# Kernel optimization log

Measured on AMD Instinct MI355X. Metric: run time of the kernel, lower is better.

## Reference

```python
import jax, jax.numpy as jnp
import numpy as np

H = 128; L = 4; N_TOTAL = 2500; M = 4; K = 12
S = N_TOTAL * M          # 10000 subgraphs
F = S * K                # 120000 flat nodes
E_INTRA = 2 * F          # 240000 intra-subgraph edges
E_INTER = 16 * N_TOTAL   # 40000 canonical edges
B = 50; VOCAB = 119; MAX_DIST = 32; BN_EPS = 1e-5


def _bn(x, g, b):
    # training-mode BatchNorm1d over rows (biased var, eps=1e-5)
    mu = x.mean(0)
    var = x.var(0)
    return (x - mu) * jax.lax.rsqrt(var + BN_EPS) * g + b


def _gine(x, ei, ea, W1, b1, W2, b2):
    # PyG GINEConv, eps=0: MLP(x + sum_{src->dst} relu(x[src] + e))
    msg = jax.nn.relu(x[ei[0]] + ea)                              # [E,H]
    agg = jax.ops.segment_sum(msg, ei[1], num_segments=x.shape[0])
    h = x + agg
    return jax.nn.relu(h @ W1 + b1) @ W2 + b2


def setup_inputs():
    key = jax.random.key(0)
    ks = list(jax.random.split(key, 32)); it = iter(ks)
    nk = lambda: next(it)
    rn = lambda shape, s=0.05: jax.random.normal(nk(), shape, dtype=jnp.float32) * s
    x_tok = jax.random.randint(nk(), (F,), 0, VOCAB)
    dist = jax.random.randint(nk(), (F,), 0, MAX_DIST + 1)
    node_ids = jax.random.randint(nk(), (F,), 0, N_TOTAL)
    node_ids = jnp.where(jax.random.uniform(nk(), (F,)) < 0.1, -1, node_ids)
    root_flat_idx = jnp.arange(S) * K
    node_ids = node_ids.at[root_flat_idx].set(jnp.arange(S) // M)  # root = canonical node
    valid = node_ids >= 0
    sub_batch = jnp.repeat(jnp.arange(S), K)
    src = jax.random.randint(nk(), (E_INTRA,), 0, F)
    dst = (src // K) * K + jax.random.randint(nk(), (E_INTRA,), 0, K)  # stay inside subgraph
    intra_ei = jnp.stack([src, dst])
    edge_index = jax.random.randint(nk(), (2, E_INTER), 0, N_TOTAL)
    batch_ids = jnp.arange(N_TOTAL) // (N_TOTAL // B)
    lp = -jax.random.uniform(nk(), (S,)) * 3.0                    # log-probs <= 0
    z = lambda *shape: jnp.zeros(shape, jnp.float32)
    o = lambda *shape: jnp.ones(shape, jnp.float32)
    return dict(
        x_tok=x_tok, dist=dist, node_ids=node_ids, valid=valid,
        sub_batch=sub_batch, root_flat_idx=root_flat_idx,
        intra_ei=intra_ei, edge_index=edge_index, batch_ids=batch_ids,
        lp=lp, ea_flat=rn((E_INTRA, H)), edge_attr=rn((E_INTER, H)),
        atom_emb=rn((VOCAB, H)), dist_emb=rn((MAX_DIST + 1, H)),
        logp_w=rn((1, H)), logp_b=z(H),
        intra_W1=rn((L, H, H)), intra_b1=z(L, H),
        intra_W2=rn((L, H, H)), intra_b2=z(L, H),
        intra_bn_g=o(L, H), intra_bn_b=z(L, H),
        self_W=rn((L, H, H)), self_b=z(L, H),
        root_W=rn((L, H, H)), root_b=z(L, H),
        inter_W1=rn((L, H, H)), inter_b1=z(L, H),
        inter_W2=rn((L, H, H)), inter_b2=z(L, H),
        inter_bn_g=o(L, H), inter_bn_b=z(L, H),
        readout_bn_g=o(H), readout_bn_b=z(H),
        alpha_pool=o(1), alpha_inter=o(1),
    )


def reference(x_tok, dist, node_ids, valid, sub_batch, root_flat_idx, intra_ei,
              edge_index, batch_ids, lp, ea_flat, edge_attr, atom_emb, dist_emb,
              logp_w, logp_b, intra_W1, intra_b1, intra_W2, intra_b2,
              intra_bn_g, intra_bn_b, self_W, self_b, root_W, root_b,
              inter_W1, inter_b1, inter_W2, inter_b2, inter_bn_g, inter_bn_b,
              readout_bn_g, readout_bn_b, alpha_pool, alpha_inter):
    valid_f = valid.astype(jnp.float32)[:, None]                  # [F,1]
    is_root_f = jnp.zeros((F, 1), jnp.float32).at[root_flat_idx].set(1.0)
    clamped_ids = jnp.maximum(node_ids, 0)
    # input encoding: atom embedding + BFS-distance PE + log-prob PE
    logp_pe = jax.nn.relu(lp[sub_batch][:, None] * logp_w[0] + logp_b)
    h = (atom_emb[x_tok] + dist_emb[dist] + logp_pe) * valid_f
    # HT inter-root weights, normalized per canonical root id
    root_ids = node_ids[root_flat_idx]                            # [S]
    rv = root_ids >= 0
    rid = jnp.maximum(root_ids, 0)
    w_un = jnp.where(rv, jnp.exp(-alpha_inter[0] * lp), 0.0)
    w_sum = jax.ops.segment_sum(w_un, rid, num_segments=N_TOTAL)
    ht_w = jnp.where(rv, w_un / (w_sum[rid] + 1e-16), 0.0)        # [S]
    for l in range(L):
        h1 = _gine(h, intra_ei, ea_flat, intra_W1[l], intra_b1[l], intra_W2[l], intra_b2[l])
        h1 = _bn(h1, intra_bn_g[l], intra_bn_b[l]) * valid_f
        h_root_bcast = h[sub_batch * K]
        h_non_root = (h @ self_W[l] + self_b[l]) + (h_root_bcast @ root_W[l] + root_b[l])
        # HT-weighted scatter of root reps to canonical nodes
        h_roots = h[root_flat_idx]                                # [S,H]
        h_root_canon = jax.ops.segment_sum(h_roots * ht_w[:, None], rid, num_segments=N_TOTAL)
        h_inter = _gine(h_root_canon, edge_index, edge_attr, inter_W1[l], inter_b1[l], inter_W2[l], inter_b2[l])
        h_inter = _bn(h_inter, inter_bn_g[l], inter_bn_b[l])
        h_inter_bcast = h_inter[clamped_ids] * valid_f
        out = is_root_f * (h1 + h_inter_bcast) + (1.0 - is_root_f) * (h1 + h_non_root)
        h = jax.nn.relu(out) * valid_f                            # dropout p=0
    # HT softmax readout over the m subgraphs of each canonical node
    h_sub = jax.ops.segment_sum(h * valid_f, sub_batch, num_segments=S)
    h_sub_2d = h_sub.reshape(N_TOTAL, M, H)
    w = jax.nn.softmax(-alpha_pool[0] * lp.reshape(N_TOTAL, M), axis=1)
    node_emb = jnp.einsum('nm,nmh->nh', w, h_sub_2d)
    node_emb = _bn(node_emb, readout_bn_g, readout_bn_b)
    return jax.ops.segment_sum(node_emb, batch_ids, num_segments=B)  # [B,H]
```

## Files before the change

### kernel.cpp

```cpp
#include <hip/hip_runtime.h>
#include <math.h>

#define H 128
#define H4 (H/4)
#define KK 12
#define MSUB 4
#define FF 120000
#define SS 10000
#define NN 2500
#define NBATCH 50
#define NLAYER 4
#define EINTRA 240000
#define EINTER 40000
#define HH (H*H)
#define BN_EPS 1e-5f
#define CAP_I 32
#define CAP_E 96
#define WLO_SHORTS 16384

typedef short short8 __attribute__((ext_vector_type(8)));
typedef float floatx4 __attribute__((ext_vector_type(4)));

__device__ __forceinline__ unsigned short f2bf_rne(float x){
  unsigned u = __float_as_uint(x);
  unsigned r = u + 0x7FFFu + ((u >> 16) & 1u);
  return (unsigned short)(r >> 16);
}


__global__ void k_zeroi(int* __restrict__ p, int n){
  int i = blockIdx.x*256 + threadIdx.x;
  if (i < n) p[i] = 0;
}


__global__ void k_bucket(const int* __restrict__ dst, int E, int* __restrict__ cnt,
                         int* __restrict__ beid, int cap){
  int e = blockIdx.x*256 + threadIdx.x;
  if (e >= E) return;
  int d = dst[e];
  int p = atomicAdd(&cnt[d], 1);
  if (p < cap) beid[(size_t)d*cap + p] = e;
}

__global__ void k_scan(const int* __restrict__ cnt, int rows, int cap,
                       int* __restrict__ rowptr, int* __restrict__ gcount){
  __shared__ int sdata[256];
  __shared__ int sbase;
  int tid = threadIdx.x;
  int r = blockIdx.x*256 + tid;
  int v = 0;
  if (r < rows){ v = cnt[r]; if (v > cap) v = cap; }
  sdata[tid] = v;
  __syncthreads();
  for (int ofs = 1; ofs < 256; ofs <<= 1){
    int t = (tid >= ofs) ? sdata[tid-ofs] : 0;
    __syncthreads();
    sdata[tid] += t;
    __syncthreads();
  }
  if (tid == 255) sbase = atomicAdd(gcount, sdata[255]);
  __syncthreads();
  if (r < rows) rowptr[r] = sbase + sdata[tid] - v;
}

__global__ void k_csr_fill(const int* __restrict__ cnt, const int* __restrict__ rowptr,
                           const int* __restrict__ beid, const int* __restrict__ src,
                           int rows, int cap, int2* __restrict__ es){
  int f = blockIdx.x*256 + threadIdx.x;
  if (f >= rows) return;
  int n = cnt[f]; if (n > cap) n = cap;
  int base = rowptr[f];
  const int* bl = beid + (size_t)f*cap;
  for (int i = 0; i < n; ++i){
    int e = bl[i];
    es[base + i] = make_int2(e, src[e]);
  }
}


__global__ void k_wprep(const float* __restrict__ iW1, const float* __restrict__ iW2,
                        const float* __restrict__ sW,  const float* __restrict__ rW,
                        const float* __restrict__ nW1, const float* __restrict__ nW2,
                        short* __restrict__ wlo){
  int mat = blockIdx.x >> 3;
  int t = (blockIdx.x & 7)*256 + threadIdx.x;
  int l = t & 63, nt = (t >> 6) & 7, ks = t >> 9;
  int layer = mat / 6, which = mat % 6;
  const float* W;
  switch (which){
    case 0: W = iW1; break; case 1: W = iW2; break; case 2: W = sW; break;
    case 3: W = rW;  break; case 4: W = nW1; break; default: W = nW2; break;
  }
  W += (size_t)layer*HH;
  short* o = wlo + (size_t)mat*WLO_SHORTS;
  int quad = l >> 4, n15 = l & 15;
  #pragma unroll
  for (int j = 0; j < 8; ++j){
    int k = ks*32 + quad*8 + j;
    int n = nt*16 + n15;
    float v = W[(size_t)k*H + n];
    unsigned short hb = f2bf_rne(v);
    float hf = __uint_as_float((unsigned)hb << 16);
    o[(ks*8 + nt)*512 + l*8 + j] = (short)f2bf_rne(v - hf);
  }
}


__global__ void k_encode(float* __restrict__ h, const int* __restrict__ xtok,
                         const int* __restrict__ dist, const int* __restrict__ nids,
                         const int* __restrict__ subb, const float* __restrict__ lp,
                         const float* __restrict__ aemb, const float* __restrict__ demb,
                         const float* __restrict__ lw, const float* __restrict__ lb){
  int idx = blockIdx.x*256 + threadIdx.x;
  if (idx >= FF*H4) return;
  int f = idx >> 5; int c = (idx & 31) << 2;
  float vf = (nids[f] >= 0) ? 1.f : 0.f;
  float l = lp[subb[f]];
  float4 a = *(const float4*)(aemb + (size_t)xtok[f]*H + c);
  float4 d = *(const float4*)(demb + (size_t)dist[f]*H + c);
  float4 w = *(const float4*)(lw + c);
  float4 b = *(const float4*)(lb + c);
  float4 o;
  o.x = (a.x + d.x + fmaxf(fmaf(l, w.x, b.x), 0.f)) * vf;
  o.y = (a.y + d.y + fmaxf(fmaf(l, w.y, b.y), 0.f)) * vf;
  o.z = (a.z + d.z + fmaxf(fmaf(l, w.z, b.z), 0.f)) * vf;
  o.w = (a.w + d.w + fmaxf(fmaf(l, w.w, b.w), 0.f)) * vf;
  *(float4*)(h + (size_t)f*H + c) = o;
}


__global__ void k_htw(const int* __restrict__ nids, const int* __restrict__ rfi,
                      const float* __restrict__ lp, const float* __restrict__ alpha,
                      float* __restrict__ htw){
  int n = blockIdx.x*256 + threadIdx.x;
  if (n >= NN) return;
  float a = alpha[0];
  float w[MSUB]; float sum = 0.f;
  #pragma unroll
  for (int m = 0; m < MSUB; ++m){
    int s = n*MSUB + m;
    int rid = nids[rfi[s]];
    float wm = (rid >= 0) ? expf(-a*lp[s]) : 0.f;
    w[m] = wm; sum += wm;
  }
  float inv = 1.f / (sum + 1e-16f);
  #pragma unroll
  for (int m = 0; m < MSUB; ++m) htw[n*MSUB + m] = w[m]*inv;
}


__global__ void k_gine_gather2(float* __restrict__ outa, const float* __restrict__ x,
                               const float* __restrict__ ea, const int* __restrict__ cnt,
                               const int* __restrict__ rowptr, const int2* __restrict__ es,
                               int rows, int cap){
  int idx = blockIdx.x*256 + threadIdx.x;
  if (idx >= rows*H4) return;
  int f = idx >> 5; int c = (idx & 31) << 2;
  float4 acc = *(const float4*)(x + (size_t)f*H + c);
  int n = cnt[f]; if (n > cap) n = cap;
  const int2* p = es + rowptr[f];
  int i = 0;
  for (; i + 2 <= n; i += 2){
    int2 e0 = p[i];
    int2 e1 = p[i+1];
    float4 x0 = *(const float4*)(x + (size_t)e0.y*H + c);
    float4 a0 = *(const float4*)(ea + (size_t)e0.x*H + c);
    float4 x1 = *(const float4*)(x + (size_t)e1.y*H + c);
    float4 a1 = *(const float4*)(ea + (size_t)e1.x*H + c);
    acc.x += fmaxf(x0.x + a0.x, 0.f) + fmaxf(x1.x + a1.x, 0.f);
    acc.y += fmaxf(x0.y + a0.y, 0.f) + fmaxf(x1.y + a1.y, 0.f);
    acc.z += fmaxf(x0.z + a0.z, 0.f) + fmaxf(x1.z + a1.z, 0.f);
    acc.w += fmaxf(x0.w + a0.w, 0.f) + fmaxf(x1.w + a1.w, 0.f);
  }
  if (i < n){
    int2 e0 = p[i];
    float4 x0 = *(const float4*)(x + (size_t)e0.y*H + c);
    float4 a0 = *(const float4*)(ea + (size_t)e0.x*H + c);
    acc.x += fmaxf(x0.x + a0.x, 0.f);
    acc.y += fmaxf(x0.y + a0.y, 0.f);
    acc.z += fmaxf(x0.z + a0.z, 0.f);
    acc.w += fmaxf(x0.w + a0.w, 0.f);
  }
  *(float4*)(outa + (size_t)f*H + c) = acc;
}


__global__ void k_canon(float* __restrict__ canon, const float* __restrict__ h,
                        const float* __restrict__ htw, const int* __restrict__ rfi){
  int idx = blockIdx.x*256 + threadIdx.x;
  if (idx >= NN*H4) return;
  int n = idx >> 5; int c = (idx & 31) << 2;
  float4 acc = make_float4(0.f,0.f,0.f,0.f);
  #pragma unroll
  for (int m = 0; m < MSUB; ++m){
    int s = n*MSUB + m;
    float w = htw[s];
    const float* p = h + (size_t)rfi[s]*H + c;
    acc.x += w*p[0]; acc.y += w*p[1]; acc.z += w*p[2]; acc.w += w*p[3];
  }
  *(float4*)(canon + (size_t)n*H + c) = acc;
}


__global__ __launch_bounds__(256, 2) void k_mm_mfma(
    const float* __restrict__ in, float* __restrict__ out, int rows,
    const float* __restrict__ W, const short* __restrict__ wlo,
    const float* __restrict__ bias, int do_relu, const int* __restrict__ gather)
{
  __shared__ __align__(16) short whi[4][8][64][8];
  int tid = threadIdx.x;
  int w = tid >> 6, l = tid & 63;
  int quad = l >> 4, n15 = l & 15;

  #pragma unroll
  for (int i = 0; i < 8; ++i){
    int c = w + (i << 2);
    int ks = c >> 3, nt = c & 7;
    #pragma unroll
    for (int j = 0; j < 8; ++j){
      int k = ks*32 + quad*8 + j;
      int n = nt*16 + n15;
      whi[ks][nt][l][j] = (short)f2bf_rne(W[(size_t)k*H + n]);
    }
  }
  __syncthreads();

  const short* wlol = wlo + l*8;

  int ngroups = (rows + 63) >> 6;
  for (int g = blockIdx.x; g < ngroups; g += gridDim.x){
    int rload = g*64 + w*16 + n15;
    bool okload = rload < rows;
    int ir = okload ? (gather ? gather[rload] : rload) : 0;
    const float* ap = in + (size_t)ir*H + quad*8;

    short8 ah[4], al[4];
    #pragma unroll
    for (int ks = 0; ks < 4; ++ks){
      float4 a0 = okload ? *(const float4*)(ap + ks*32 + 0) : make_float4(0.f,0.f,0.f,0.f);
      float4 a1 = okload ? *(const float4*)(ap + ks*32 + 4) : make_float4(0.f,0.f,0.f,0.f);
      float av[8] = {a0.x,a0.y,a0.z,a0.w,a1.x,a1.y,a1.z,a1.w};
      #pragma unroll
      for (int j = 0; j < 8; ++j){
        unsigned short hb = f2bf_rne(av[j]);
        float hf = __uint_as_float((unsigned)hb << 16);
        ah[ks][j] = (short)hb;
        al[ks][j] = (short)f2bf_rne(av[j] - hf);
      }
    }

    floatx4 acc[8] = {};
    #pragma unroll
    for (int ks = 0; ks < 4; ++ks){
      #pragma unroll
      for (int nt = 0; nt < 8; ++nt){
        short8 bh = *(const short8*)&whi[ks][nt][l][0];
        short8 bl = *(const short8*)(wlol + (ks*8 + nt)*512);
        acc[nt] = __builtin_amdgcn_mfma_f32_16x16x32_bf16(ah[ks], bh, acc[nt], 0, 0, 0);
        acc[nt] = __builtin_amdgcn_mfma_f32_16x16x32_bf16(al[ks], bh, acc[nt], 0, 0, 0);
        acc[nt] = __builtin_amdgcn_mfma_f32_16x16x32_bf16(ah[ks], bl, acc[nt], 0, 0, 0);
      }
    }

    int rbase = g*64 + w*16 + quad*4;
    #pragma unroll
    for (int nt = 0; nt < 8; ++nt){
      int col = nt*16 + n15;
      float bv = bias[col];
      #pragma unroll
      for (int reg = 0; reg < 4; ++reg){
        int r = rbase + reg;
        if (r < rows){
          float v = acc[nt][reg] + bv;
          if (do_relu) v = fmaxf(v, 0.f);
          out[(size_t)r*H + col] = v;
        }
      }
    }
  }
}


__global__ __launch_bounds__(256, 2) void k_mm_mfma_stats(
    const float* __restrict__ in, float* __restrict__ out, int rows,
    const float* __restrict__ W, const short* __restrict__ wlo,
    const float* __restrict__ bias, double* __restrict__ part)
{
  __shared__ __align__(16) short whi[4][8][64][8];
  int tid = threadIdx.x;
  int w = tid >> 6, l = tid & 63;
  int quad = l >> 4, n15 = l & 15;

  #pragma unroll
  for (int i = 0; i < 8; ++i){
    int c = w + (i << 2);
    int ks = c >> 3, nt = c & 7;
    #pragma unroll
    for (int j = 0; j < 8; ++j){
      int k = ks*32 + quad*8 + j;
      int n = nt*16 + n15;
      whi[ks][nt][l][j] = (short)f2bf_rne(W[(size_t)k*H + n]);
    }
  }
  __syncthreads();

  const short* wlol = wlo + l*8;

  float s0[8] = {0,0,0,0,0,0,0,0};
  float s1[8] = {0,0,0,0,0,0,0,0};

  int ngroups = (rows + 63) >> 6;
  for (int g = blockIdx.x; g < ngroups; g += gridDim.x){
    int rload = g*64 + w*16 + n15;
    bool okload = rload < rows;
    const float* ap = in + (size_t)(okload ? rload : 0)*H + quad*8;

    short8 ah[4], al[4];
    #pragma unroll
    for (int ks = 0; ks < 4; ++ks){
      float4 a0 = okload ? *(const float4*)(ap + ks*32 + 0) : make_float4(0.f,0.f,0.f,0.f);
      float4 a1 = okload ? *(const float4*)(ap + ks*32 + 4) : make_float4(0.f,0.f,0.f,0.f);
      float av[8] = {a0.x,a0.y,a0.z,a0.w,a1.x,a1.y,a1.z,a1.w};
      #pragma unroll
      for (int j = 0; j < 8; ++j){
        unsigned short hb = f2bf_rne(av[j]);
        float hf = __uint_as_float((unsigned)hb << 16);
        ah[ks][j] = (short)hb;
        al[ks][j] = (short)f2bf_rne(av[j] - hf);
      }
    }

    floatx4 acc[8] = {};
    #pragma unroll
    for (int ks = 0; ks < 4; ++ks){
      #pragma unroll
      for (int nt = 0; nt < 8; ++nt){
        short8 bh = *(const short8*)&whi[ks][nt][l][0];
        short8 bl = *(const short8*)(wlol + (ks*8 + nt)*512);
        acc[nt] = __builtin_amdgcn_mfma_f32_16x16x32_bf16(ah[ks], bh, acc[nt], 0, 0, 0);
        acc[nt] = __builtin_amdgcn_mfma_f32_16x16x32_bf16(al[ks], bh, acc[nt], 0, 0, 0);
        acc[nt] = __builtin_amdgcn_mfma_f32_16x16x32_bf16(ah[ks], bl, acc[nt], 0, 0, 0);
      }
    }

    int rbase = g*64 + w*16 + quad*4;
    #pragma unroll
    for (int nt = 0; nt < 8; ++nt){
      int col = nt*16 + n15;
      float bv = bias[col];
      #pragma unroll
      for (int reg = 0; reg < 4; ++reg){
        int r = rbase + reg;
        if (r < rows){
          float v = acc[nt][reg] + bv;
          out[(size_t)r*H + col] = v;
          s0[nt] += v;
          s1[nt] += v*v;
        }
      }
    }
  }

  __syncthreads();
  double* red = (double*)&whi[0][0][0][0];
  #pragma unroll
  for (int nt = 0; nt < 8; ++nt){
    float a = s0[nt], b = s1[nt];
    a += __shfl_xor(a, 16, 64); b += __shfl_xor(b, 16, 64);
    a += __shfl_xor(a, 32, 64); b += __shfl_xor(b, 32, 64);
    if (quad == 0){
      int col = nt*16 + n15;
      red[(size_t)(w*2+0)*H + col] = (double)a;
      red[(size_t)(w*2+1)*H + col] = (double)b;
    }
  }
  __syncthreads();
  if (tid < H){
    int col = tid;
    double a = red[0*H+col] + red[2*H+col] + red[4*H+col] + red[6*H+col];
    double b = red[1*H+col] + red[3*H+col] + red[5*H+col] + red[7*H+col];
    part[(size_t)(blockIdx.x*2+0)*H + col] = a;
    part[(size_t)(blockIdx.x*2+1)*H + col] = b;
  }
}


__global__ void k_bnstats_p(const float* __restrict__ x, int rows, double* __restrict__ part){
  int g = blockIdx.x*256 + threadIdx.x;
  int c = g & (H-1);
  int s = g >> 7;
  int stride = (gridDim.x*256) >> 7;
  double a = 0.0, b = 0.0;
  for (int r = s; r < rows; r += stride){
    float v = x[(size_t)r*H + c];
    a += v; b += (double)v*(double)v;
  }
  part[(size_t)(s*2+0)*H + c] = a;
  part[(size_t)(s*2+1)*H + c] = b;
}

__global__ void k_bnfin_par(const double* __restrict__ part, int nstreams, int rows,
                            float* __restrict__ muinv){
  __shared__ double sh0[256], sh1[256];
  int c = blockIdx.x;
  int tid = threadIdx.x;
  double a = 0.0, b = 0.0;
  for (int s = tid; s < nstreams; s += 256){
    a += part[(size_t)(s*2+0)*H + c];
    b += part[(size_t)(s*2+1)*H + c];
  }
  sh0[tid] = a; sh1[tid] = b;
  __syncthreads();
  for (int ofs = 128; ofs > 0; ofs >>= 1){
    if (tid < ofs){ sh0[tid] += sh0[tid+ofs]; sh1[tid] += sh1[tid+ofs]; }
    __syncthreads();
  }
  if (tid == 0){
    double mu = sh0[0] / (double)rows;
    double var = sh1[0] / (double)rows - mu*mu;
    muinv[c]   = (float)mu;
    muinv[H+c] = (float)(1.0 / sqrt(var + (double)BN_EPS));
  }
}

__global__ void k_bnapply(float* __restrict__ x, const float* __restrict__ muinv,
                          const float* __restrict__ g, const float* __restrict__ b, int rows){
  int idx = blockIdx.x*256 + threadIdx.x;
  if (idx >= rows*H4) return;
  int r = idx >> 5; int c = (idx & 31) << 2;
  float4 v  = *(const float4*)(x + (size_t)r*H + c);
  float4 mu = *(const float4*)(muinv + c);
  float4 iv = *(const float4*)(muinv + H + c);
  float4 gg = *(const float4*)(g + c);
  float4 bb = *(const float4*)(b + c);
  v.x = (v.x-mu.x)*iv.x*gg.x + bb.x;
  v.y = (v.y-mu.y)*iv.y*gg.y + bb.y;
  v.z = (v.z-mu.z)*iv.z*gg.z + bb.z;
  v.w = (v.w-mu.w)*iv.w*gg.w + bb.w;
  *(float4*)(x + (size_t)r*H + c) = v;
}


__global__ void k_combine(float* __restrict__ h, const float* __restrict__ h1raw,
                          const float* __restrict__ r1, const float* __restrict__ r2,
                          const float* __restrict__ hinter, const float* __restrict__ muinv,
                          const float* __restrict__ bg, const float* __restrict__ bb,
                          const int* __restrict__ nids){
  int idx = blockIdx.x*256 + threadIdx.x;
  if (idx >= FF*H4) return;
  int f = idx >> 5; int c = (idx & 31) << 2;
  int nid = nids[f];
  float vf = (nid >= 0) ? 1.f : 0.f;
  int cid = (nid < 0) ? 0 : nid;
  float4 x  = *(const float4*)(h1raw + (size_t)f*H + c);
  float4 mu = *(const float4*)(muinv + c);
  float4 iv = *(const float4*)(muinv + H + c);
  float4 g4 = *(const float4*)(bg + c);
  float4 b4 = *(const float4*)(bb + c);
  float4 h1;
  h1.x = ((x.x-mu.x)*iv.x*g4.x + b4.x) * vf;
  h1.y = ((x.y-mu.y)*iv.y*g4.y + b4.y) * vf;
  h1.z = ((x.z-mu.z)*iv.z*g4.z + b4.z) * vf;
  h1.w = ((x.w-mu.w)*iv.w*g4.w + b4.w) * vf;
  float4 o;
  if (f % KK == 0){
    float4 hi = *(const float4*)(hinter + (size_t)cid*H + c);
    o.x = h1.x + hi.x*vf; o.y = h1.y + hi.y*vf; o.z = h1.z + hi.z*vf; o.w = h1.w + hi.w*vf;
  } else {
    float4 a  = *(const float4*)(r1 + (size_t)f*H + c);
    float4 rr = *(const float4*)(r2 + (size_t)(f/KK)*H + c);
    o.x = h1.x + a.x + rr.x; o.y = h1.y + a.y + rr.y; o.z = h1.z + a.z + rr.z; o.w = h1.w + a.w + rr.w;
  }
  o.x = fmaxf(o.x,0.f)*vf; o.y = fmaxf(o.y,0.f)*vf; o.z = fmaxf(o.z,0.f)*vf; o.w = fmaxf(o.w,0.f)*vf;
  *(float4*)(h + (size_t)f*H + c) = o;
}


__global__ void k_hsub(float* __restrict__ hsub, const float* __restrict__ h){
  int idx = blockIdx.x*256 + threadIdx.x;
  if (idx >= SS*H4) return;
  int s = idx >> 5; int c = (idx & 31) << 2;
  float4 acc = make_float4(0.f,0.f,0.f,0.f);
  const float* base = h + (size_t)s*KK*H + c;
  #pragma unroll
  for (int k = 0; k < KK; ++k){
    float4 v = *(const float4*)(base + (size_t)k*H);
    acc.x += v.x; acc.y += v.y; acc.z += v.z; acc.w += v.w;
  }
  *(float4*)(hsub + (size_t)s*H + c) = acc;
}

__global__ void k_poolw(float* __restrict__ poolw, const float* __restrict__ lp,
                        const float* __restrict__ alpha){
  int n = blockIdx.x*256 + threadIdx.x;
  if (n >= NN) return;
  float a = alpha[0];
  float s0 = -a*lp[n*MSUB+0], s1 = -a*lp[n*MSUB+1], s2 = -a*lp[n*MSUB+2], s3 = -a*lp[n*MSUB+3];
  float m = fmaxf(fmaxf(s0,s1), fmaxf(s2,s3));
  float e0 = expf(s0-m), e1 = expf(s1-m), e2 = expf(s2-m), e3 = expf(s3-m);
  float sum = e0+e1+e2+e3;
  poolw[n*MSUB+0] = e0/sum; poolw[n*MSUB+1] = e1/sum;
  poolw[n*MSUB+2] = e2/sum; poolw[n*MSUB+3] = e3/sum;
}

__global__ void k_nodeemb(float* __restrict__ nemb, const float* __restrict__ hsub,
                          const float* __restrict__ poolw){
  int idx = blockIdx.x*256 + threadIdx.x;
  if (idx >= NN*H4) return;
  int n = idx >> 5; int c = (idx & 31) << 2;
  float w0 = poolw[n*MSUB+0], w1 = poolw[n*MSUB+1], w2 = poolw[n*MSUB+2], w3 = poolw[n*MSUB+3];
  const float* base = hsub + (size_t)n*MSUB*H + c;
  float4 v0 = *(const float4*)(base + 0*H);
  float4 v1 = *(const float4*)(base + 1*H);
  float4 v2 = *(const float4*)(base + 2*H);
  float4 v3 = *(const float4*)(base + 3*H);
  float4 o;
  o.x = w0*v0.x + w1*v1.x + w2*v2.x + w3*v3.x;
  o.y = w0*v0.y + w1*v1.y + w2*v2.y + w3*v3.y;
  o.z = w0*v0.z + w1*v1.z + w2*v2.z + w3*v3.z;
  o.w = w0*v0.w + w1*v1.w + w2*v2.w + w3*v3.w;
  *(float4*)(nemb + (size_t)n*H + c) = o;
}

__global__ void k_out(float* __restrict__ out, const float* __restrict__ nemb,
                      const float* __restrict__ muinv, const float* __restrict__ g,
                      const float* __restrict__ b){
  int idx = blockIdx.x*256 + threadIdx.x;
  if (idx >= NBATCH*H) return;
  int bi = idx >> 7; int c = idx & (H-1);
  float mu = muinv[c], iv = muinv[H+c], gg = g[c], bb = b[c];
  float acc = 0.f;
  const float* base = nemb + (size_t)bi*(NN/NBATCH)*H + c;
  for (int i = 0; i < NN/NBATCH; ++i)
    acc += (base[(size_t)i*H] - mu)*iv*gg + bb;
  out[idx] = acc;
}


extern "C" void kernel_launch(void* const* d_in, const int* in_sizes, int n_in,
                              void* d_out, int out_size, void* d_ws, size_t ws_size,
                              hipStream_t stream) {
  const int*   x_tok      = (const int*)  d_in[0];
  const int*   dist       = (const int*)  d_in[1];
  const int*   node_ids   = (const int*)  d_in[2];
  const int*   sub_batch  = (const int*)  d_in[4];
  const int*   rfi        = (const int*)  d_in[5];
  const int*   intra_ei   = (const int*)  d_in[6];
  const int*   edge_index = (const int*)  d_in[7];
  const float* lp         = (const float*)d_in[9];
  const float* ea_flat    = (const float*)d_in[10];
  const float* edge_attr  = (const float*)d_in[11];
  const float* atom_emb   = (const float*)d_in[12];
  const float* dist_emb   = (const float*)d_in[13];
  const float* logp_w     = (const float*)d_in[14];
  const float* logp_b     = (const float*)d_in[15];
  const float* intra_W1   = (const float*)d_in[16];
  const float* intra_b1   = (const float*)d_in[17];
  const float* intra_W2   = (const float*)d_in[18];
  const float* intra_b2   = (const float*)d_in[19];
  const float* intra_bn_g = (const float*)d_in[20];
  const float* intra_bn_b = (const float*)d_in[21];
  const float* self_W     = (const float*)d_in[22];
  const float* self_b     = (const float*)d_in[23];
  const float* root_W     = (const float*)d_in[24];
  const float* root_b     = (const float*)d_in[25];
  const float* inter_W1   = (const float*)d_in[26];
  const float* inter_b1   = (const float*)d_in[27];
  const float* inter_W2   = (const float*)d_in[28];
  const float* inter_b2   = (const float*)d_in[29];
  const float* inter_bn_g = (const float*)d_in[30];
  const float* inter_bn_b = (const float*)d_in[31];
  const float* ro_bn_g    = (const float*)d_in[32];
  const float* ro_bn_b    = (const float*)d_in[33];
  const float* alpha_pool = (const float*)d_in[34];
  const float* alpha_inter= (const float*)d_in[35];

  const int* isrc = intra_ei;
  const int* idst = intra_ei + EINTRA;
  const int* esrc = edge_index;
  const int* edst = edge_index + EINTER;

  float* out = (float*)d_out;

  char* ws = (char*)d_ws;
  size_t off = 0;
  auto nxt = [&](size_t bytes) -> void* {
    void* p = ws + off;
    off += (bytes + 255) & ~(size_t)255;
    return p;
  };
  const int G_MM_F = 1024;
  const int G_MM_S = (SS + 63)/64;
  const int G_MM_N = (NN + 63)/64;
  const int G_BN_S = 32;

  float*  h      = (float*) nxt((size_t)FF*H*4);
  float*  hmid   = (float*) nxt((size_t)FF*H*4);
  float*  tbuf   = (float*) nxt((size_t)FF*H*4);
  float*  r2     = (float*) nxt((size_t)SS*H*4);
  float*  canon  = (float*) nxt((size_t)NN*H*4);
  float*  agg2   = (float*) nxt((size_t)NN*H*4);
  float*  hsub   = (float*) nxt((size_t)SS*H*4);
  float*  nemb   = (float*) nxt((size_t)NN*H*4);
  float*  htw    = (float*) nxt((size_t)SS*4);
  float*  poolw  = (float*) nxt((size_t)NN*MSUB*4);
  double* statsA = (double*)nxt((size_t)G_MM_F*2*H*8);
  double* statsB = (double*)nxt((size_t)(G_BN_S*2)*2*H*8);
  float*  muinvA = (float*) nxt((size_t)2*H*4);
  float*  muinvB = (float*) nxt((size_t)2*H*4);
  short*  wloG   = (short*) nxt((size_t)24*WLO_SHORTS*2);
  int*    icnt   = (int*)   nxt((size_t)FF*4);
  int*    ibeid  = (int*)   nxt((size_t)FF*CAP_I*4);
  int*    ecnt   = (int*)   nxt((size_t)NN*4);
  int*    ebeid  = (int*)   nxt((size_t)NN*CAP_E*4);
  int*    irow   = (int*)   nxt((size_t)FF*4);
  int*    erow   = (int*)   nxt((size_t)NN*4);
  int2*   ies    = (int2*)  nxt((size_t)EINTRA*8);
  int2*   ees    = (int2*)  nxt((size_t)EINTER*8);
  int*    gcnt   = (int*)   nxt((size_t)2*4);
  (void)ws_size; (void)n_in; (void)in_sizes; (void)out_size; (void)sub_batch;

  const int G_FH4 = FF*H4/256;
  const int G_SH4 = SS*H4/256;
  const int G_NH4 = (NN*H4 + 255)/256;
  const int G_N   = (NN + 255)/256;
  const int G_F   = (FF + 255)/256;

  k_zeroi<<<G_F, 256, 0, stream>>>(icnt, FF);
  k_zeroi<<<G_N, 256, 0, stream>>>(ecnt, NN);
  k_zeroi<<<1, 256, 0, stream>>>(gcnt, 2);

  k_wprep<<<24*8, 256, 0, stream>>>(intra_W1, intra_W2, self_W, root_W,
                                    inter_W1, inter_W2, wloG);

  k_bucket<<<(EINTRA+255)/256, 256, 0, stream>>>(idst, EINTRA, icnt, ibeid, CAP_I);
  k_bucket<<<(EINTER+255)/256, 256, 0, stream>>>(edst, EINTER, ecnt, ebeid, CAP_E);
  k_scan<<<G_F, 256, 0, stream>>>(icnt, FF, CAP_I, irow, gcnt);
  k_scan<<<G_N, 256, 0, stream>>>(ecnt, NN, CAP_E, erow, gcnt+1);
  k_csr_fill<<<G_F, 256, 0, stream>>>(icnt, irow, ibeid, isrc, FF, CAP_I, ies);
  k_csr_fill<<<G_N, 256, 0, stream>>>(ecnt, erow, ebeid, esrc, NN, CAP_E, ees);

  k_encode<<<G_FH4, 256, 0, stream>>>(h, x_tok, dist, node_ids, sub_batch, lp,
                                      atom_emb, dist_emb, logp_w, logp_b);
  k_htw<<<G_N, 256, 0, stream>>>(node_ids, rfi, lp, alpha_inter, htw);

  for (int l = 0; l < NLAYER; ++l){
    const float* W1 = intra_W1 + (size_t)l*HH;
    const float* W2 = intra_W2 + (size_t)l*HH;
    const short* lo_iW1 = wloG + (size_t)(l*6+0)*WLO_SHORTS;
    const short* lo_iW2 = wloG + (size_t)(l*6+1)*WLO_SHORTS;
    const short* lo_sW  = wloG + (size_t)(l*6+2)*WLO_SHORTS;
    const short* lo_rW  = wloG + (size_t)(l*6+3)*WLO_SHORTS;
    const short* lo_nW1 = wloG + (size_t)(l*6+4)*WLO_SHORTS;
    const short* lo_nW2 = wloG + (size_t)(l*6+5)*WLO_SHORTS;

    k_gine_gather2<<<G_FH4, 256, 0, stream>>>(hmid, h, ea_flat, icnt, irow, ies, FF, CAP_I);
    k_mm_mfma<<<G_MM_F, 256, 0, stream>>>(hmid, tbuf, FF, W1, lo_iW1,
                                          intra_b1 + (size_t)l*H, 1, nullptr);
    k_mm_mfma_stats<<<G_MM_F, 256, 0, stream>>>(tbuf, hmid, FF, W2, lo_iW2,
                                                intra_b2 + (size_t)l*H, statsA);
    k_bnfin_par<<<H, 256, 0, stream>>>(statsA, G_MM_F, FF, muinvA);

    k_canon<<<G_NH4, 256, 0, stream>>>(canon, h, htw, rfi);
    k_mm_mfma<<<G_MM_S, 256, 0, stream>>>(h, r2, SS, root_W + (size_t)l*HH, lo_rW,
                                          root_b + (size_t)l*H, 0, rfi);

    k_gine_gather2<<<G_NH4, 256, 0, stream>>>(agg2, canon, edge_attr, ecnt, erow, ees, NN, CAP_E);
    k_mm_mfma<<<G_MM_N, 256, 0, stream>>>(agg2, tbuf, NN, inter_W1 + (size_t)l*HH, lo_nW1,
                                          inter_b1 + (size_t)l*H, 1, nullptr);
    k_mm_mfma<<<G_MM_N, 256, 0, stream>>>(tbuf, agg2, NN, inter_W2 + (size_t)l*HH, lo_nW2,
                                          inter_b2 + (size_t)l*H, 0, nullptr);
    k_bnstats_p<<<G_BN_S, 256, 0, stream>>>(agg2, NN, statsB);
    k_bnfin_par<<<H, 256, 0, stream>>>(statsB, G_BN_S*2, NN, muinvB);
    k_bnapply<<<G_NH4, 256, 0, stream>>>(agg2, muinvB, inter_bn_g + (size_t)l*H,
                                         inter_bn_b + (size_t)l*H, NN);

    k_mm_mfma<<<G_MM_F, 256, 0, stream>>>(h, tbuf, FF, self_W + (size_t)l*HH, lo_sW,
                                          self_b + (size_t)l*H, 0, nullptr);
    k_combine<<<G_FH4, 256, 0, stream>>>(h, hmid, tbuf, r2, agg2, muinvA,
                                         intra_bn_g + (size_t)l*H,
                                         intra_bn_b + (size_t)l*H, node_ids);
  }

  k_hsub<<<G_SH4, 256, 0, stream>>>(hsub, h);
  k_poolw<<<G_N, 256, 0, stream>>>(poolw, lp, alpha_pool);
  k_nodeemb<<<G_NH4, 256, 0, stream>>>(nemb, hsub, poolw);
  k_bnstats_p<<<G_BN_S, 256, 0, stream>>>(nemb, NN, statsB);
  k_bnfin_par<<<H, 256, 0, stream>>>(statsB, G_BN_S*2, NN, muinvB);
  k_out<<<(NBATCH*H+255)/256, 256, 0, stream>>>(out, nemb, muinvB, ro_bn_g, ro_bn_b);
}
```

Baseline: 2.060 ms.

## Fuse intra MLP GEMMs and self-linear with combine, precompute bf16 hi weights

Fuses the two intra-GINE MLP GEMMs into one kernel that keeps the ReLU intermediate in per-wave LDS, which removes the full F x H temporary buffer and its round trip through global memory. The self-linear GEMM is fused with the combine/BN-apply step so its output never goes to global memory. The hi bf16 weight fragments are now precomputed once in k_wprep and read from global, instead of being rebuilt into LDS in every block. In-place read and write of h in the self-combine kernel relies on each wave finishing its reads of a row before writing it, and the fused kernels assume the row count is a multiple of 64.

After: 2.940 ms. +42.8%, slower.

```diff
diff --git a/kernel.cpp b/kernel.cpp
--- a/kernel.cpp
+++ b/kernel.cpp
@@ -16,7 +16,8 @@
 #define BN_EPS 1e-5f
 #define CAP_I 32
 #define CAP_E 96
-#define WLO_SHORTS 16384
+#define WF_SHORTS 16384
+#define ZPAD 132
 
 typedef short short8 __attribute__((ext_vector_type(8)));
 typedef float floatx4 __attribute__((ext_vector_type(4)));
@@ -82,7 +83,7 @@
 __global__ void k_wprep(const float* __restrict__ iW1, const float* __restrict__ iW2,
                         const float* __restrict__ sW,  const float* __restrict__ rW,
                         const float* __restrict__ nW1, const float* __restrict__ nW2,
-                        short* __restrict__ wlo){
+                        short* __restrict__ whiG, short* __restrict__ wloG){
   int mat = blockIdx.x >> 3;
   int t = (blockIdx.x & 7)*256 + threadIdx.x;
   int l = t & 63, nt = (t >> 6) & 7, ks = t >> 9;
@@ -93,7 +94,8 @@
     case 3: W = rW;  break; case 4: W = nW1; break; default: W = nW2; break;
   }
   W += (size_t)layer*HH;
-  short* o = wlo + (size_t)mat*WLO_SHORTS;
+  short* oh = whiG + (size_t)mat*WF_SHORTS;
+  short* ol = wloG + (size_t)mat*WF_SHORTS;
   int quad = l >> 4, n15 = l & 15;
   #pragma unroll
   for (int j = 0; j < 8; ++j){
@@ -102,7 +104,9 @@
     float v = W[(size_t)k*H + n];
     unsigned short hb = f2bf_rne(v);
     float hf = __uint_as_float((unsigned)hb << 16);
-    o[(ks*8 + nt)*512 + l*8 + j] = (short)f2bf_rne(v - hf);
+    int idx = (ks*8 + nt)*512 + l*8 + j;
+    oh[idx] = (short)hb;
+    ol[idx] = (short)f2bf_rne(v - hf);
   }
 }
 
@@ -203,30 +207,42 @@
 }
 
 
+__device__ __forceinline__ void conv8(const float* av, short8& ah, short8& al){
+  #pragma unroll
+  for (int j = 0; j < 8; ++j){
+    unsigned short hb = f2bf_rne(av[j]);
+    float hf = __uint_as_float((unsigned)hb << 16);
+    ah[j] = (short)hb;
+    al[j] = (short)f2bf_rne(av[j] - hf);
+  }
+}
+
+__device__ __forceinline__ void mfma3(floatx4* acc, const short8* ah, const short8* al,
+                                      const short* hp, const short* lp){
+  #pragma unroll
+  for (int ks = 0; ks < 4; ++ks){
+    #pragma unroll
+    for (int nt = 0; nt < 8; ++nt){
+      short8 bh = *(const short8*)(hp + (ks*8 + nt)*512);
+      short8 bl = *(const short8*)(lp + (ks*8 + nt)*512);
+      acc[nt] = __builtin_amdgcn_mfma_f32_16x16x32_bf16(ah[ks], bh, acc[nt], 0, 0, 0);
+      acc[nt] = __builtin_amdgcn_mfma_f32_16x16x32_bf16(al[ks], bh, acc[nt], 0, 0, 0);
+      acc[nt] = __builtin_amdgcn_mfma_f32_16x16x32_bf16(ah[ks], bl, acc[nt], 0, 0, 0);
+    }
+  }
+}
+
+
 __global__ __launch_bounds__(256, 2) void k_mm_mfma(
     const float* __restrict__ in, float* __restrict__ out, int rows,
-    const float* __restrict__ W, const short* __restrict__ wlo,
+    const short* __restrict__ whi, const short* __restrict__ wlo,
     const float* __restrict__ bias, int do_relu, const int* __restrict__ gather)
 {
-  __shared__ __align__(16) short whi[4][8][64][8];
   int tid = threadIdx.x;
   int w = tid >> 6, l = tid & 63;
   int quad = l >> 4, n15 = l & 15;
-
-  #pragma unroll
-  for (int i = 0; i < 8; ++i){
-    int c = w + (i << 2);
-    int ks = c >> 3, nt = c & 7;
-    #pragma unroll
-    for (int j = 0; j < 8; ++j){
-      int k = ks*32 + quad*8 + j;
-      int n = nt*16 + n15;
-      whi[ks][nt][l][j] = (short)f2bf_rne(W[(size_t)k*H + n]);
-    }
-  }
-  __syncthreads();
-
-  const short* wlol = wlo + l*8;
+  const short* hp = whi + l*8;
+  const short* lp = wlo + l*8;
 
   int ngroups = (rows + 63) >> 6;
   for (int g = blockIdx.x; g < ngroups; g += gridDim.x){
@@ -241,27 +257,11 @@
       float4 a0 = okload ? *(const float4*)(ap + ks*32 + 0) : make_float4(0.f,0.f,0.f,0.f);
       float4 a1 = okload ? *(const float4*)(ap + ks*32 + 4) : make_float4(0.f,0.f,0.f,0.f);
       float av[8] = {a0.x,a0.y,a0.z,a0.w,a1.x,a1.y,a1.z,a1.w};
-      #pragma unroll
-      for (int j = 0; j < 8; ++j){
-        unsigned short hb = f2bf_rne(av[j]);
-        float hf = __uint_as_float((unsigned)hb << 16);
-        ah[ks][j] = (short)hb;
-        al[ks][j] = (short)f2bf_rne(av[j] - hf);
-      }
+      conv8(av, ah[ks], al[ks]);
     }
 
     floatx4 acc[8] = {};
-    #pragma unroll
-    for (int ks = 0; ks < 4; ++ks){
-      #pragma unroll
-      for (int nt = 0; nt < 8; ++nt){
-        short8 bh = *(const short8*)&whi[ks][nt][l][0];
-        short8 bl = *(const short8*)(wlol + (ks*8 + nt)*512);
-        acc[nt] = __builtin_amdgcn_mfma_f32_16x16x32_bf16(ah[ks], bh, acc[nt], 0, 0, 0);
-        acc[nt] = __builtin_amdgcn_mfma_f32_16x16x32_bf16(al[ks], bh, acc[nt], 0, 0, 0);
-        acc[nt] = __builtin_amdgcn_mfma_f32_16x16x32_bf16(ah[ks], bl, acc[nt], 0, 0, 0);
-      }
-    }
+    mfma3(acc, ah, al, hp, lp);
 
     int rbase = g*64 + w*16 + quad*4;
     #pragma unroll
@@ -282,88 +282,83 @@
 }
 
 
-__global__ __launch_bounds__(256, 2) void k_mm_mfma_stats(
-    const float* __restrict__ in, float* __restrict__ out, int rows,
-    const float* __restrict__ W, const short* __restrict__ wlo,
-    const float* __restrict__ bias, double* __restrict__ part)
+__global__ __launch_bounds__(256, 2) void k_mlp_fused(
+    float* __restrict__ x, int rows,
+    const short* __restrict__ whi1, const short* __restrict__ wlo1, const float* __restrict__ b1,
+    const short* __restrict__ whi2, const short* __restrict__ wlo2, const float* __restrict__ b2,
+    double* __restrict__ part)
 {
-  __shared__ __align__(16) short whi[4][8][64][8];
+  __shared__ float zb[4][16][ZPAD];
   int tid = threadIdx.x;
   int w = tid >> 6, l = tid & 63;
   int quad = l >> 4, n15 = l & 15;
-
-  #pragma unroll
-  for (int i = 0; i < 8; ++i){
-    int c = w + (i << 2);
-    int ks = c >> 3, nt = c & 7;
-    #pragma unroll
-    for (int j = 0; j < 8; ++j){
-      int k = ks*32 + quad*8 + j;
-      int n = nt*16 + n15;
-      whi[ks][nt][l][j] = (short)f2bf_rne(W[(size_t)k*H + n]);
-    }
-  }
-  __syncthreads();
-
-  const short* wlol = wlo + l*8;
+  const short* h1 = whi1 + l*8; const short* l1 = wlo1 + l*8;
+  const short* h2 = whi2 + l*8; const short* l2 = wlo2 + l*8;
+  float (*Z)[ZPAD] = zb[w];
 
   float s0[8] = {0,0,0,0,0,0,0,0};
   float s1[8] = {0,0,0,0,0,0,0,0};
 
-  int ngroups = (rows + 63) >> 6;
+  int ngroups = rows >> 6;
   for (int g = blockIdx.x; g < ngroups; g += gridDim.x){
-    int rload = g*64 + w*16 + n15;
-    bool okload = rload < rows;
-    const float* ap = in + (size_t)(okload ? rload : 0)*H + quad*8;
-
+    const float* ap = x + (size_t)(g*64 + w*16 + n15)*H + quad*8;
     short8 ah[4], al[4];
     #pragma unroll
     for (int ks = 0; ks < 4; ++ks){
-      float4 a0 = okload ? *(const float4*)(ap + ks*32 + 0) : make_float4(0.f,0.f,0.f,0.f);
-      float4 a1 = okload ? *(const float4*)(ap + ks*32 + 4) : make_float4(0.f,0.f,0.f,0.f);
+      float4 a0 = *(const float4*)(ap + ks*32 + 0);
+      float4 a1 = *(const float4*)(ap + ks*32 + 4);
       float av[8] = {a0.x,a0.y,a0.z,a0.w,a1.x,a1.y,a1.z,a1.w};
+      conv8(av, ah[ks], al[ks]);
+    }
+
+    floatx4 acc[8] = {};
+    mfma3(acc, ah, al, h1, l1);
+
+    #pragma unroll
+    for (int nt = 0; nt < 8; ++nt){
+      float bv = b1[nt*16 + n15];
       #pragma unroll
-      for (int j = 0; j < 8; ++j){
-        unsigned short hb = f2bf_rne(av[j]);
-        float hf = __uint_as_float((unsigned)hb << 16);
-        ah[ks][j] = (short)hb;
-        al[ks][j] = (short)f2bf_rne(av[j] - hf);
-      }
-    }
-
-    floatx4 acc[8] = {};
+      for (int reg = 0; reg < 4; ++reg)
+        Z[quad*4 + reg][nt*16 + n15] = fmaxf(acc[nt][reg] + bv, 0.f);
+    }
+
     #pragma unroll
     for (int ks = 0; ks < 4; ++ks){
-      #pragma unroll
-      for (int nt = 0; nt < 8; ++nt){
-        short8 bh = *(const short8*)&whi[ks][nt][l][0];
-        short8 bl = *(const short8*)(wlol + (ks*8 + nt)*512);
-        acc[nt] = __builtin_amdgcn_mfma_f32_16x16x32_bf16(ah[ks], bh, acc[nt], 0, 0, 0);
-        acc[nt] = __builtin_amdgcn_mfma_f32_16x16x32_bf16(al[ks], bh, acc[nt], 0, 0, 0);
-        acc[nt] = __builtin_amdgcn_mfma_f32_16x16x32_bf16(ah[ks], bl, acc[nt], 0, 0, 0);
-      }
-    }
-
-    int rbase = g*64 + w*16 + quad*4;
+      float4 z0 = *(const float4*)&Z[n15][ks*32 + quad*8 + 0];
+      float4 z1 = *(const float4*)&Z[n15][ks*32 + quad*8 + 4];
+      float av[8] = {z0.x,z0.y,z0.z,z0.w,z1.x,z1.y,z1.z,z1.w};
+      conv8(av, ah[ks], al[ks]);
+    }
+
+    floatx4 acc2[8] = {};
+    mfma3(acc2, ah, al, h2, l2);
+
     #pragma unroll
     for (int nt = 0; nt < 8; ++nt){
-      int col = nt*16 + n15;
-      float bv = bias[col];
+      float bv = b2[nt*16 + n15];
       #pragma unroll
       for (int reg = 0; reg < 4; ++reg){
-        int r = rbase + reg;
-        if (r < rows){
-          float v = acc[nt][reg] + bv;
-          out[(size_t)r*H + col] = v;
-          s0[nt] += v;
-          s1[nt] += v*v;
-        }
+        float v = acc2[nt][reg] + bv;
+        s0[nt] += v;
+        s1[nt] += v*v;
+        Z[quad*4 + reg][nt*16 + n15] = v;
       }
     }
+
+    #pragma unroll
+    for (int ii = 0; ii < 2; ++ii){
+      int row = (l >> 3) + 8*ii;
+      float* orow = x + (size_t)(g*64 + w*16 + row)*H;
+      #pragma unroll
+      for (int jj = 0; jj < 4; ++jj){
+        int c4 = ((l & 7) + 8*jj)*4;
+        *(float4*)(orow + c4) = *(const float4*)&Z[row][c4];
+      }
+    }
   }
 
   __syncthreads();
-  double* red = (double*)&whi[0][0][0][0];
+  double* red = (double*)&zb[0][0][0];
   #pragma unroll
   for (int nt = 0; nt < 8; ++nt){
     float a = s0[nt], b = s1[nt];
@@ -382,6 +377,91 @@
     double b = red[1*H+col] + red[3*H+col] + red[5*H+col] + red[7*H+col];
     part[(size_t)(blockIdx.x*2+0)*H + col] = a;
     part[(size_t)(blockIdx.x*2+1)*H + col] = b;
+  }
+}
+
+
+__global__ __launch_bounds__(256, 2) void k_selfcombine(
+    float* __restrict__ h, int rows,
+    const short* __restrict__ whiS, const short* __restrict__ wloS, const float* __restrict__ biasS,
+    const float* __restrict__ hmid, const float* __restrict__ r2,
+    const float* __restrict__ agg2, const float* __restrict__ muinv,
+    const float* __restrict__ bng, const float* __restrict__ bnb,
+    const int* __restrict__ nids)
+{
+  __shared__ float zb[4][16][ZPAD];
+  int tid = threadIdx.x;
+  int w = tid >> 6, l = tid & 63;
+  int quad = l >> 4, n15 = l & 15;
+  const short* hp = whiS + l*8;
+  const short* lp = wloS + l*8;
+  float (*Z)[ZPAD] = zb[w];
+
+  int ngroups = rows >> 6;
+  for (int g = blockIdx.x; g < ngroups; g += gridDim.x){
+    const float* ap = h + (size_t)(g*64 + w*16 + n15)*H + quad*8;
+    short8 ah[4], al[4];
+    #pragma unroll
+    for (int ks = 0; ks < 4; ++ks){
+      float4 a0 = *(const float4*)(ap + ks*32 + 0);
+      float4 a1 = *(const float4*)(ap + ks*32 + 4);
+      float av[8] = {a0.x,a0.y,a0.z,a0.w,a1.x,a1.y,a1.z,a1.w};
+      conv8(av, ah[ks], al[ks]);
+    }
+
+    floatx4 acc[8] = {};
+    mfma3(acc, ah, al, hp, lp);
+
+    #pragma unroll
+    for (int nt = 0; nt < 8; ++nt){
+      float bv = biasS[nt*16 + n15];
+      #pragma unroll
+      for (int reg = 0; reg < 4; ++reg)
+        Z[quad*4 + reg][nt*16 + n15] = acc[nt][reg] + bv;
+    }
+
+    #pragma unroll
+    for (int ii = 0; ii < 2; ++ii){
+      int row = (l >> 3) + 8*ii;
+      int r = g*64 + w*16 + row;
+      int nid = nids[r];
+      float vf = (nid >= 0) ? 1.f : 0.f;
+      int cid = (nid < 0) ? 0 : nid;
+      bool isroot = (r % KK) == 0;
+      int rs = r / KK;
+      const float* hmrow = hmid + (size_t)r*H;
+      const float* r2row = r2 + (size_t)rs*H;
+      const float* hirow = agg2 + (size_t)cid*H;
+      float* orow = h + (size_t)r*H;
+      #pragma unroll
+      for (int jj = 0; jj < 4; ++jj){
+        int c4 = ((l & 7) + 8*jj)*4;
+        float4 hm = *(const float4*)(hmrow + c4);
+        float4 mu = *(const float4*)(muinv + c4);
+        float4 iv = *(const float4*)(muinv + H + c4);
+        float4 g4 = *(const float4*)(bng + c4);
+        float4 b4 = *(const float4*)(bnb + c4);
+        float4 h1;
+        h1.x = ((hm.x-mu.x)*iv.x*g4.x + b4.x) * vf;
+        h1.y = ((hm.y-mu.y)*iv.y*g4.y + b4.y) * vf;
+        h1.z = ((hm.z-mu.z)*iv.z*g4.z + b4.z) * vf;
+        h1.w = ((hm.w-mu.w)*iv.w*g4.w + b4.w) * vf;
+        float4 o;
+        if (isroot){
+          float4 hi = *(const float4*)(hirow + c4);
+          o.x = h1.x + hi.x*vf; o.y = h1.y + hi.y*vf;
+          o.z = h1.z + hi.z*vf; o.w = h1.w + hi.w*vf;
+        } else {
+          float4 r1 = *(const float4*)&Z[row][c4];
+          float4 rr = *(const float4*)(r2row + c4);
+          o.x = h1.x + r1.x + rr.x; o.y = h1.y + r1.y + rr.y;
+          o.z = h1.z + r1.z + rr.z; o.w = h1.w + r1.w + rr.w;
+        }
+        o.x = fmaxf(o.x,0.f)*vf; o.y = fmaxf(o.y,0.f)*vf;
+        o.z = fmaxf(o.z,0.f)*vf; o.w = fmaxf(o.w,0.f)*vf;
+        *(float4*)(orow + c4) = o;
+      }
+    }
   }
 }
 
@@ -439,41 +519,6 @@
   v.z = (v.z-mu.z)*iv.z*gg.z + bb.z;
   v.w = (v.w-mu.w)*iv.w*gg.w + bb.w;
   *(float4*)(x + (size_t)r*H + c) = v;
-}
-
-
-__global__ void k_combine(float* __restrict__ h, const float* __restrict__ h1raw,
-                          const float* __restrict__ r1, const float* __restrict__ r2,
-                          const float* __restrict__ hinter, const float* __restrict__ muinv,
-                          const float* __restrict__ bg, const float* __restrict__ bb,
-                          const int* __restrict__ nids){
-  int idx = blockIdx.x*256 + threadIdx.x;
-  if (idx >= FF*H4) return;
-  int f = idx >> 5; int c = (idx & 31) << 2;
-  int nid = nids[f];
-  float vf = (nid >= 0) ? 1.f : 0.f;
-  int cid = (nid < 0) ? 0 : nid;
-  float4 x  = *(const float4*)(h1raw + (size_t)f*H + c);
-  float4 mu = *(const float4*)(muinv + c);
-  float4 iv = *(const float4*)(muinv + H + c);
-  float4 g4 = *(const float4*)(bg + c);
-  float4 b4 = *(const float4*)(bb + c);
-  float4 h1;
-  h1.x = ((x.x-mu.x)*iv.x*g4.x + b4.x) * vf;
-  h1.y = ((x.y-mu.y)*iv.y*g4.y + b4.y) * vf;
-  h1.z = ((x.z-mu.z)*iv.z*g4.z + b4.z) * vf;
-  h1.w = ((x.w-mu.w)*iv.w*g4.w + b4.w) * vf;
-  float4 o;
-  if (f % KK == 0){
-    float4 hi = *(const float4*)(hinter + (size_t)cid*H + c);
-    o.x = h1.x + hi.x*vf; o.y = h1.y + hi.y*vf; o.z = h1.z + hi.z*vf; o.w = h1.w + hi.w*vf;
-  } else {
-    float4 a  = *(const float4*)(r1 + (size_t)f*H + c);
-    float4 rr = *(const float4*)(r2 + (size_t)(f/KK)*H + c);
-    o.x = h1.x + a.x + rr.x; o.y = h1.y + a.y + rr.y; o.z = h1.z + a.z + rr.z; o.w = h1.w + a.w + rr.w;
-  }
-  o.x = fmaxf(o.x,0.f)*vf; o.y = fmaxf(o.y,0.f)*vf; o.z = fmaxf(o.z,0.f)*vf; o.w = fmaxf(o.w,0.f)*vf;
-  *(float4*)(h + (size_t)f*H + c) = o;
 }
 
 
@@ -597,10 +642,10 @@
 
   float*  h      = (float*) nxt((size_t)FF*H*4);
   float*  hmid   = (float*) nxt((size_t)FF*H*4);
-  float*  tbuf   = (float*) nxt((size_t)FF*H*4);
   float*  r2     = (float*) nxt((size_t)SS*H*4);
   float*  canon  = (float*) nxt((size_t)NN*H*4);
   float*  agg2   = (float*) nxt((size_t)NN*H*4);
+  float*  tbufN  = (float*) nxt((size_t)NN*H*4);
   float*  hsub   = (float*) nxt((size_t)SS*H*4);
   float*  nemb   = (float*) nxt((size_t)NN*H*4);
   float*  htw    = (float*) nxt((size_t)SS*4);
@@ -609,7 +654,8 @@
   double* statsB = (double*)nxt((size_t)(G_BN_S*2)*2*H*8);
   float*  muinvA = (float*) nxt((size_t)2*H*4);
   float*  muinvB = (float*) nxt((size_t)2*H*4);
-  short*  wloG   = (short*) nxt((size_t)24*WLO_SHORTS*2);
+  short*  whiG   = (short*) nxt((size_t)24*WF_SHORTS*2);
+  short*  wloG   = (short*) nxt((size_t)24*WF_SHORTS*2);
   int*    icnt   = (int*)   nxt((size_t)FF*4);
   int*    ibeid  = (int*)   nxt((size_t)FF*CAP_I*4);
   int*    ecnt   = (int*)   nxt((size_t)NN*4);
@@ -632,7 +678,7 @@
   k_zeroi<<<1, 256, 0, stream>>>(gcnt, 2);
 
   k_wprep<<<24*8, 256, 0, stream>>>(intra_W1, intra_W2, self_W, root_W,
-                                    inter_W1, inter_W2, wloG);
+                                    inter_W1, inter_W2, whiG, wloG);
 
   k_bucket<<<(EINTRA+255)/256, 256, 0, stream>>>(idst, EINTRA, icnt, ibeid, CAP_I);
   k_bucket<<<(EINTER+255)/256, 256, 0, stream>>>(edst, EINTER, ecnt, ebeid, CAP_E);
@@ -646,41 +692,43 @@
   k_htw<<<G_N, 256, 0, stream>>>(node_ids, rfi, lp, alpha_inter, htw);
 
   for (int l = 0; l < NLAYER; ++l){
-    const float* W1 = intra_W1 + (size_t)l*HH;
-    const float* W2 = intra_W2 + (size_t)l*HH;
-    const short* lo_iW1 = wloG + (size_t)(l*6+0)*WLO_SHORTS;
-    const short* lo_iW2 = wloG + (size_t)(l*6+1)*WLO_SHORTS;
-    const short* lo_sW  = wloG + (size_t)(l*6+2)*WLO_SHORTS;
-    const short* lo_rW  = wloG + (size_t)(l*6+3)*WLO_SHORTS;
-    const short* lo_nW1 = wloG + (size_t)(l*6+4)*WLO_SHORTS;
-    const short* lo_nW2 = wloG + (size_t)(l*6+5)*WLO_SHORTS;
+    const short* hi_iW1 = whiG + (size_t)(l*6+0)*WF_SHORTS;
+    const short* hi_iW2 = whiG + (size_t)(l*6+1)*WF_SHORTS;
+    const short* hi_sW  = whiG + (size_t)(l*6+2)*WF_SHORTS;
+    const short* hi_rW  = whiG + (size_t)(l*6+3)*WF_SHORTS;
+    const short* hi_nW1 = whiG + (size_t)(l*6+4)*WF_SHORTS;
+    const short* hi_nW2 = whiG + (size_t)(l*6+5)*WF_SHORTS;
+    const short* lo_iW1 = wloG + (size_t)(l*6+0)*WF_SHORTS;
+    const short* lo_iW2 = wloG + (size_t)(l*6+1)*WF_SHORTS;
+    const short* lo_sW  = wloG + (size_t)(l*6+2)*WF_SHORTS;
+    const short* lo_rW  = wloG + (size_t)(l*6+3)*WF_SHORTS;
+    const short* lo_nW1 = wloG + (size_t)(l*6+4)*WF_SHORTS;
+    const short* lo_nW2 = wloG + (size_t)(l*6+5)*WF_SHORTS;
 
     k_gine_gather2<<<G_FH4, 256, 0, stream>>>(hmid, h, ea_flat, icnt, irow, ies, FF, CAP_I);
-    k_mm_mfma<<<G_MM_F, 256, 0, stream>>>(hmid, tbuf, FF, W1, lo_iW1,
-                                          intra_b1 + (size_t)l*H, 1, nullptr);
-    k_mm_mfma_stats<<<G_MM_F, 256, 0, stream>>>(tbuf, hmid, FF, W2, lo_iW2,
-                                                intra_b2 + (size_t)l*H, statsA);
+    k_mlp_fused<<<G_MM_F, 256, 0, stream>>>(hmid, FF,
+                                            hi_iW1, lo_iW1, intra_b1 + (size_t)l*H,
+                                            hi_iW2, lo_iW2, intra_b2 + (size_t)l*H, statsA);
     k_bnfin_par<<<H, 256, 0, stream>>>(statsA, G_MM_F, FF, muinvA);
 
     k_canon<<<G_NH4, 256, 0, stream>>>(canon, h, htw, rfi);
-    k_mm_mfma<<<G_MM_S, 256, 0, stream>>>(h, r2, SS, root_W + (size_t)l*HH, lo_rW,
+    k_mm_mfma<<<G_MM_S, 256, 0, stream>>>(h, r2, SS, hi_rW, lo_rW,
                                           root_b + (size_t)l*H, 0, rfi);
 
     k_gine_gather2<<<G_NH4, 256, 0, stream>>>(agg2, canon, edge_attr, ecnt, erow, ees, NN, CAP_E);
-    k_mm_mfma<<<G_MM_N, 256, 0, stream>>>(agg2, tbuf, NN, inter_W1 + (size_t)l*HH, lo_nW1,
+    k_mm_mfma<<<G_MM_N, 256, 0, stream>>>(agg2, tbufN, NN, hi_nW1, lo_nW1,
                                           inter_b1 + (size_t)l*H, 1, nullptr);
-    k_mm_mfma<<<G_MM_N, 256, 0, stream>>>(tbuf, agg2, NN, inter_W2 + (size_t)l*HH, lo_nW2,
+    k_mm_mfma<<<G_MM_N, 256, 0, stream>>>(tbufN, agg2, NN, hi_nW2, lo_nW2,
                                           inter_b2 + (size_t)l*H, 0, nullptr);
     k_bnstats_p<<<G_BN_S, 256, 0, stream>>>(agg2, NN, statsB);
     k_bnfin_par<<<H, 256, 0, stream>>>(statsB, G_BN_S*2, NN, muinvB);
     k_bnapply<<<G_NH4, 256, 0, stream>>>(agg2, muinvB, inter_bn_g + (size_t)l*H,
                                          inter_bn_b + (size_t)l*H, NN);
 
-    k_mm_mfma<<<G_MM_F, 256, 0, stream>>>(h, tbuf, FF, self_W + (size_t)l*HH, lo_sW,
-                                          self_b + (size_t)l*H, 0, nullptr);
-    k_combine<<<G_FH4, 256, 0, stream>>>(h, hmid, tbuf, r2, agg2, muinvA,
-                                         intra_bn_g + (size_t)l*H,
-                                         intra_bn_b + (size_t)l*H, node_ids);
+    k_selfcombine<<<G_MM_F, 256, 0, stream>>>(h, FF, hi_sW, lo_sW,
+                                              self_b + (size_t)l*H, hmid, r2, agg2,
+                                              muinvA, intra_bn_g + (size_t)l*H,
+                                              intra_bn_b + (size_t)l*H, node_ids);
   }
 
   k_hsub<<<G_SH4, 256, 0, stream>>>(hsub, h);
```
